# Kernel tuning notes

Measured on AMD Instinct MI355X. Metric: run time of the kernel, lower is better.

## Reference

```python
import jax, jax.numpy as jnp
import numpy as np

# Module hyperparameters (match init_kwargs)
C = 64      # in_channels
O = 256     # out_channels
K = 3       # filter_size
SUB = 2     # subsampling
SIGMA = 1.0
SCALE = 1.0 / SIGMA ** 2
EPS = 1e-8


def setup_inputs() -> dict:
    key = jax.random.key(0)
    k1, k2 = jax.random.split(key)
    x = jax.random.normal(k1, (32, C, 64, 64), dtype=jnp.float32)
    weight = jax.random.normal(k2, (O, C * K * K), dtype=jnp.float32)
    return {"x": x, "weight": weight}


def reference(x, weight):
    # Faithful to CKNLayer.forward, but expressed as a direct convolution
    # instead of materializing the im2col (unfold) tensor:
    #   unfold -> per-patch L2 norm -> (patches/norm) @ w_norm.T
    # == conv(x, w_norm) / patch_norm,   patch_norm = sqrt(conv(x^2, ones))
    B, _, H, W = x.shape
    pad = K // 2

    # F.normalize(weight, p=2, dim=1): clamp norm at 1e-12
    w_norm = weight / jnp.maximum(
        jnp.linalg.norm(weight, axis=1, keepdims=True), 1e-12
    )
    # torch unfold orders patch features as (c, kh, kw) -> reshape matches
    w4 = w_norm.reshape(O, C, K, K)

    dn = jax.lax.conv_dimension_numbers(x.shape, w4.shape, ('NCHW', 'OIHW', 'NCHW'))
    dots = jax.lax.conv_general_dilated(
        x, w4, window_strides=(1, 1), padding=[(pad, pad), (pad, pad)],
        dimension_numbers=dn)  # [B, O, H, W]

    ones_k = jnp.ones((1, C, K, K), x.dtype)
    sq = jax.lax.conv_general_dilated(
        x * x, ones_k, window_strides=(1, 1), padding=[(pad, pad), (pad, pad)],
        dimension_numbers=dn)  # [B, 1, H, W] = sum of squares per patch
    patch_norm = jnp.sqrt(jnp.maximum(sq, 0.0)) + EPS

    # Gaussian RBF on the unit sphere: exp(scale * (cos_sim - 1))
    out = jnp.exp(SCALE * (dots / patch_norm - 1.0))  # [B, O, H, W]

    # avg_pool2d(kernel=SUB, stride=SUB), H, W divisible by SUB
    out = out.reshape(B, O, H // SUB, SUB, W // SUB, SUB).mean(axis=(3, 5))
    return out
```

## Files before the change

### kernel.cpp

```cpp
#include <hip/hip_runtime.h>
#include <hip/hip_bf16.h>

typedef __attribute__((ext_vector_type(8))) short bf16x8;
typedef __attribute__((ext_vector_type(4))) float f32x4;
typedef __attribute__((ext_vector_type(16))) float f32x16;
typedef __attribute__((ext_vector_type(4))) unsigned u32x4;

__device__ __forceinline__ unsigned bfbits(float v) {
  __hip_bfloat16 h = __float2bfloat16(v);
  return (unsigned)*reinterpret_cast<unsigned short*>(&h);
}

__global__ void wnorm_kernel(const float* __restrict__ w,
                             ushort* __restrict__ wt,
                             ushort* __restrict__ wt3) {
  const int o = blockIdx.x;
  const int c = threadIdx.x;
  float v[9];
  float ss = 0.f;
  const float* row = w + o * 576 + c * 9;
#pragma unroll
  for (int j = 0; j < 9; ++j) { v[j] = row[j]; ss += v[j] * v[j]; }
#pragma unroll
  for (int off = 32; off > 0; off >>= 1) ss += __shfl_xor(ss, off);
  const float inv = 1.0f / fmaxf(sqrtf(ss), 1e-12f);
  const int g = o >> 5, n = o & 31;
#pragma unroll
  for (int j = 0; j < 9; ++j) {
    const ushort bv = (ushort)bfbits(v[j] * inv);
    wt[o * 576 + j * 64 + c] = bv;
    const int ks = j * 4 + (c >> 4);
    wt3[((ks * 8 + g) * 32 + n) * 16 + (c & 15)] = bv;
  }
}

__global__ __launch_bounds__(256, 8) void xprep_kernel(
    const float* __restrict__ x, ushort* __restrict__ xt,
    float* __restrict__ css) {
  __shared__ __align__(16) unsigned tile[64 * 33];
  __shared__ __align__(16) float cssp[4 * 64];
  const int t = threadIdx.x;
  const int y = blockIdx.x, b = blockIdx.y;
  const int c = t >> 2, m = t & 3;
  const int lane = t & 63, w = t >> 6;

  const float* src = x + (((size_t)b * 64 + c) * 64 + y) * 64 + m * 4;
  float f[16];
#pragma unroll
  for (int j4 = 0; j4 < 4; ++j4) {
    const f32x4 v = *(const f32x4*)(src + j4 * 16);
#pragma unroll
    for (int k = 0; k < 4; ++k) f[j4 * 4 + k] = v[k];
  }
  float s[16];
#pragma unroll
  for (int j = 0; j < 16; ++j) {
    float v = f[j] * f[j];
    v += __shfl_xor(v, 4);
    v += __shfl_xor(v, 8);
    v += __shfl_xor(v, 16);
    v += __shfl_xor(v, 32);
    s[j] = v;
  }
  if (lane < 4) {
#pragma unroll
    for (int j4 = 0; j4 < 4; ++j4) {
      f32x4 v = {s[j4 * 4], s[j4 * 4 + 1], s[j4 * 4 + 2], s[j4 * 4 + 3]};
      *(f32x4*)(cssp + w * 64 + j4 * 16 + lane * 4) = v;
    }
  }
  const int parity = c & 1;
  const int c2 = c >> 1;
#pragma unroll
  for (int j = 0; j < 16; ++j) {
    const float pf = __shfl_xor(f[j], 4);
    const bool mine = parity ? (j >= 8) : (j < 8);
    if (mine) {
      const unsigned dw = parity ? (bfbits(pf) | (bfbits(f[j]) << 16))
                                 : (bfbits(f[j]) | (bfbits(pf) << 16));
      const int px = (j >> 2) * 16 + m * 4 + (j & 3);
      tile[px * 33 + c2] = dw;
    }
  }
  __syncthreads();
  {
    const int xr = t >> 2, q = t & 3;
    unsigned d[8];
#pragma unroll
    for (int i = 0; i < 8; ++i) d[i] = tile[xr * 33 + q * 8 + i];
    ushort* dst = xt + (((size_t)b * 64 + y) * 64 + xr) * 64 + q * 16;
    u32x4 v0 = {d[0], d[1], d[2], d[3]};
    u32x4 v1 = {d[4], d[5], d[6], d[7]};
    *(u32x4*)dst = v0;
    *(u32x4*)(dst + 8) = v1;
  }
  if (t < 64) {
    const float sum = cssp[t] + cssp[64 + t] + cssp[128 + t] + cssp[192 + t];
    css[((size_t)b * 64 + y) * 64 + t] = sum;
  }
}

__global__ void invp_kernel(const float* __restrict__ css,
                            float* __restrict__ invp) {
  const int xx = threadIdx.x;
  const int y = blockIdx.x, b = blockIdx.y;
  float s = 0.f;
#pragma unroll
  for (int dy = -1; dy <= 1; ++dy) {
    const int yy = y + dy;
    if ((unsigned)yy < 64u) s += css[((size_t)b * 64 + yy) * 64 + xx];
  }
  const float sl = __shfl_up(s, 1);
  const float sr = __shfl_down(s, 1);
  const float tot = s + ((xx > 0) ? sl : 0.f) + ((xx < 63) ? sr : 0.f);
  invp[((size_t)b * 64 + y) * 64 + xx] =
      1.0f / (sqrtf(fmaxf(tot, 0.f)) + 1e-8f);
}

__global__ __launch_bounds__(512, 4) void ckn_main(
    const ushort* __restrict__ xt, const float* __restrict__ invp_g,
    const ushort* __restrict__ wt3, float* __restrict__ out) {
  __shared__ __align__(16) char smem[37376];
  char* const xs = smem;
  float* const pool = (float*)smem;
  float* const invp = (float*)(smem + 36864);

  const int tid = threadIdx.x;
  const int y0 = blockIdx.x;
  const int b = blockIdx.y;

  if (tid < 64) {
    const int r4 = tid >> 4, colsel = (tid >> 3) & 1, cblk = tid & 7;
    *(f32x4*)(xs + r4 * 8448 + colsel * 65 * 128 + cblk * 16) =
        (f32x4){0.f, 0.f, 0.f, 0.f};
  }
  if (tid < 128)
    invp[tid] = invp_g[((size_t)b * 64 + 2 * y0 + (tid >> 6)) * 64 + (tid & 63)];

  {
    const int xx = tid >> 3;
    const int c0 = 8 * ((tid & 7) ^ ((xx + 1) & 7));
    const ushort* srcb = xt + ((size_t)b * 64) * 4096 + (size_t)xx * 64 + c0;
#pragma unroll
    for (int r4 = 0; r4 < 4; ++r4) {
      const int y_img = 2 * y0 - 1 + r4;
      char* dst = xs + r4 * 8448 + 128 + tid * 16;
      if ((unsigned)y_img < 64u) {
        const ushort* src = srcb + (size_t)y_img * 4096;
        __builtin_amdgcn_global_load_lds(
            (const __attribute__((address_space(1))) void*)src,
            (__attribute__((address_space(3))) void*)dst, 16, 0, 0);
      } else {
        *(f32x4*)dst = (f32x4){0.f, 0.f, 0.f, 0.f};
      }
    }
  }

  const int lane = tid & 63;
  const int wid = tid >> 6;
  const int wave_m = wid & 1;
  const int wave_n = wid >> 1;
  const int lane31 = lane & 31;
  const int hi = lane >> 5;

  const ushort* wb3 = wt3 + (size_t)lane31 * 16 + hi * 8;
  const int g0 = wave_n * 2;

  bf16x8 bq[2][2];
#pragma unroll
  for (int nf = 0; nf < 2; ++nf) {
    bq[0][nf] = *(const bf16x8*)(wb3 + (size_t)(0 * 8 + g0 + nf) * 512);
    bq[1][nf] = *(const bf16x8*)(wb3 + (size_t)(1 * 8 + g0 + nf) * 512);
  }

  __syncthreads();

  f32x16 acc[2][2];
#pragma unroll
  for (int i = 0; i < 2; ++i)
#pragma unroll
    for (int j = 0; j < 2; ++j)
#pragma unroll
      for (int e = 0; e < 16; ++e) acc[i][j][e] = 0.f;

#pragma unroll
  for (int ks = 0; ks < 36; ++ks) {
    const int t9 = ks >> 2;
    const int kh = t9 / 3, kw = t9 % 3;
    const int cb = (ks & 3) * 32 + hi * 16;
    const int r4 = wave_m + kh;
    const int cur = ks & 1;
    bf16x8 afrag[2];
#pragma unroll
    for (int mf = 0; mf < 2; ++mf) {
      const int col = mf * 32 + lane31 + kw;
      const int addr = r4 * 8448 + col * 128 + (cb ^ ((col & 7) << 4));
      afrag[mf] = *(const bf16x8*)(xs + addr);
    }
    __builtin_amdgcn_s_setprio(1);
#pragma unroll
    for (int mf = 0; mf < 2; ++mf)
#pragma unroll
      for (int nf = 0; nf < 2; ++nf)
        acc[mf][nf] = __builtin_amdgcn_mfma_f32_32x32x16_bf16(
            afrag[mf], bq[cur][nf], acc[mf][nf], 0, 0, 0);
    __builtin_amdgcn_s_setprio(0);
    if (ks + 2 < 36) {
#pragma unroll
      for (int nf = 0; nf < 2; ++nf)
        bq[cur][nf] =
            *(const bf16x8*)(wb3 + (size_t)((ks + 2) * 8 + g0 + nf) * 512);
    }
  }

  float ep[2][2][4][2];
#pragma unroll
  for (int mf = 0; mf < 2; ++mf) {
#pragma unroll
    for (int q = 0; q < 4; ++q) {
      const f32x4 ip =
          *(const f32x4*)(invp + wave_m * 64 + mf * 32 + 8 * q + 4 * hi);
#pragma unroll
      for (int nf = 0; nf < 2; ++nf) {
        const float e0 = __expf(acc[mf][nf][4 * q + 0] * ip[0] - 1.f);
        const float e1 = __expf(acc[mf][nf][4 * q + 1] * ip[1] - 1.f);
        const float e2 = __expf(acc[mf][nf][4 * q + 2] * ip[2] - 1.f);
        const float e3 = __expf(acc[mf][nf][4 * q + 3] * ip[3] - 1.f);
        ep[mf][nf][q][0] = e0 + e1;
        ep[mf][nf][q][1] = e2 + e3;
      }
    }
  }
  __syncthreads();

  if (wave_m == 1) {
#pragma unroll
    for (int mf = 0; mf < 2; ++mf)
#pragma unroll
      for (int nf = 0; nf < 2; ++nf)
#pragma unroll
        for (int q = 0; q < 4; ++q) {
          const int o = wave_n * 64 + nf * 32 + lane31;
          const int px = mf * 16 + 4 * q + 2 * hi;
          *(float2*)(pool + o * 36 + px) =
              make_float2(ep[mf][nf][q][0], ep[mf][nf][q][1]);
        }
  }
  __syncthreads();
  if (wave_m == 0) {
#pragma unroll
    for (int mf = 0; mf < 2; ++mf)
#pragma unroll
      for (int nf = 0; nf < 2; ++nf)
#pragma unroll
        for (int q = 0; q < 4; ++q) {
          const int o = wave_n * 64 + nf * 32 + lane31;
          const int px = mf * 16 + 4 * q + 2 * hi;
          float2* p = (float2*)(pool + o * 36 + px);
          const float2 othr = *p;
          *p = make_float2(0.25f * (ep[mf][nf][q][0] + othr.x),
                           0.25f * (ep[mf][nf][q][1] + othr.y));
        }
  }
  __syncthreads();

  const size_t obase = (((size_t)b * 256) * 32 + y0) * 32;
#pragma unroll
  for (int j = 0; j < 4; ++j) {
    const int o = j * 64 + (tid >> 3);
    const int ch = (tid & 7) * 4;
    const f32x4 v = *(const f32x4*)(pool + o * 36 + ch);
    *(f32x4*)(out + obase + (size_t)o * 1024 + ch) = v;
  }
}

__global__ __launch_bounds__(512, 4) void ckn_main_v1(
    const float* __restrict__ x, const ushort* __restrict__ wt,
    float* __restrict__ out) {
  __shared__ __align__(16) char smem[43552];
  char* const xs = smem;
  float* const invp = (float*)(smem + 33792);
  float* const cs = (float*)(smem + 34304);
  float* const csp = (float*)(smem + 35360);
  float* const pool = (float*)smem;

  const int tid = threadIdx.x;
  const int y0 = blockIdx.x;
  const int b = blockIdx.y;

  if (tid < 64) {
    const int r4 = tid >> 4, colsel = (tid >> 3) & 1, cblk = tid & 7;
    const int col = colsel * 65;
    *(f32x4*)(xs + r4 * 8448 + col * 128 + cblk * 16) =
        (f32x4){0.f, 0.f, 0.f, 0.f};
  }
  {
    const int xx = tid & 63;
    const int cg = tid >> 6;
    const int col = xx + 1;
    const int sw = (cg * 16) ^ ((col & 7) << 4);
#pragma unroll
    for (int r4 = 0; r4 < 4; ++r4) {
      const int y_img = 2 * y0 - 1 + r4;
      char* dst = xs + r4 * 8448 + col * 128 + sw;
      if ((unsigned)y_img < 64u) {
        const float* src =
            x + (((size_t)b * 64 + cg * 8) * 64 + y_img) * 64 + xx;
        float ss = 0.f;
        union { bf16x8 v; ushort u[8]; } pk;
#pragma unroll
        for (int j = 0; j < 8; ++j) {
          const float f = src[(size_t)j * 4096];
          ss += f * f;
          pk.u[j] = (ushort)bfbits(f);
        }
        *(bf16x8*)dst = pk.v;
        csp[(r4 * 8 + cg) * 64 + xx] = ss;
      } else {
        *(bf16x8*)dst = (bf16x8){0, 0, 0, 0, 0, 0, 0, 0};
        csp[(r4 * 8 + cg) * 64 + xx] = 0.f;
      }
    }
  }
  __syncthreads();
  if (tid < 256) {
    const int r4 = tid >> 6, xc = tid & 63;
    float s = 0.f;
#pragma unroll
    for (int cg = 0; cg < 8; ++cg) s += csp[(r4 * 8 + cg) * 64 + xc];
    cs[r4 * 66 + xc + 1] = s;
  }
  if (tid >= 256 && tid < 264) {
    const int t = tid - 256;
    cs[(t >> 1) * 66 + (t & 1) * 65] = 0.f;
  }
  __syncthreads();
  if (tid < 128) {
    const int ry = tid >> 6, xp = tid & 63;
    float s = 0.f;
#pragma unroll
    for (int dr = 0; dr < 3; ++dr)
#pragma unroll
      for (int dc = 0; dc < 3; ++dc) s += cs[(ry + dr) * 66 + xp + dc];
    invp[tid] = 1.0f / (sqrtf(fmaxf(s, 0.f)) + 1e-8f);
  }
  __syncthreads();

  const int lane = tid & 63;
  const int wid = tid >> 6;
  const int wave_m = wid & 1;
  const int wave_n = wid >> 1;
  const int lane16 = lane & 15;
  const int klane = lane >> 4;
  const int o_base = wave_n * 64;

  f32x4 acc[4][4];
#pragma unroll
  for (int i = 0; i < 4; ++i)
#pragma unroll
    for (int j = 0; j < 4; ++j) acc[i][j] = (f32x4){0.f, 0.f, 0.f, 0.f};
  const ushort* wbase = wt + (o_base + lane16) * 576 + klane * 8;
#pragma unroll
  for (int ks = 0; ks < 18; ++ks) {
    const int t9 = ks >> 1;
    const int kh = t9 / 3, kw = t9 % 3;
    const int cb = (ks & 1) * 64 + klane * 16;
    bf16x8 bfrag[4];
#pragma unroll
    for (int fn = 0; fn < 4; ++fn)
      bfrag[fn] = *(const bf16x8*)(wbase + fn * 16 * 576 + ks * 32);
    const int r4 = wave_m + kh;
#pragma unroll
    for (int fm = 0; fm < 4; ++fm) {
      const int col = fm * 16 + lane16 + kw;
      const int addr = r4 * 8448 + col * 128 + (cb ^ ((col & 7) << 4));
      const bf16x8 afrag = *(const bf16x8*)(xs + addr);
#pragma unroll
      for (int fn = 0; fn < 4; ++fn)
        acc[fm][fn] = __builtin_amdgcn_mfma_f32_16x16x32_bf16(
            afrag, bfrag[fn], acc[fm][fn], 0, 0, 0);
    }
  }
  float ep0[4][4], ep1[4][4];
#pragma unroll
  for (int fm = 0; fm < 4; ++fm) {
    const int m = wave_m * 64 + fm * 16 + klane * 4;
    const f32x4 ip = *(const f32x4*)(invp + m);
#pragma unroll
    for (int fn = 0; fn < 4; ++fn) {
      const f32x4 v = acc[fm][fn];
      const float e0 = __expf(v[0] * ip[0] - 1.f);
      const float e1 = __expf(v[1] * ip[1] - 1.f);
      const float e2 = __expf(v[2] * ip[2] - 1.f);
      const float e3 = __expf(v[3] * ip[3] - 1.f);
      ep0[fm][fn] = e0 + e1;
      ep1[fm][fn] = e2 + e3;
    }
  }
  __syncthreads();
  if (wave_m == 1) {
#pragma unroll
    for (int fm = 0; fm < 4; ++fm) {
      const int ox = fm * 8 + klane * 2;
#pragma unroll
      for (int fn = 0; fn < 4; ++fn) {
        const int o = o_base + fn * 16 + lane16;
        *(float2*)(pool + o * 32 + ox) = make_float2(ep0[fm][fn], ep1[fm][fn]);
      }
    }
  }
  __syncthreads();
  if (wave_m == 0) {
#pragma unroll
    for (int fm = 0; fm < 4; ++fm) {
      const int ox = fm * 8 + klane * 2;
#pragma unroll
      for (int fn = 0; fn < 4; ++fn) {
        const int o = o_base + fn * 16 + lane16;
        const float2 othr = *(const float2*)(pool + o * 32 + ox);
        const float r0 = 0.25f * (ep0[fm][fn] + othr.x);
        const float r1 = 0.25f * (ep1[fm][fn] + othr.y);
        *(float2*)(out + ((((size_t)b * 256 + o) * 32 + y0) * 32 + ox)) =
            make_float2(r0, r1);
      }
    }
  }
}

extern "C" void kernel_launch(void* const* d_in, const int* in_sizes, int n_in,
                              void* d_out, int out_size, void* d_ws,
                              size_t ws_size, hipStream_t stream) {
  const float* x = (const float*)d_in[0];
  const float* w = (const float*)d_in[1];
  float* out = (float*)d_out;

  const size_t XT_BYTES = 32ull * 64 * 64 * 64 * 2;
  const size_t CSS_BYTES = 32ull * 64 * 64 * 4;
  const size_t WT_BYTES = 256ull * 576 * 2;
  const size_t NEED = XT_BYTES + 2 * CSS_BYTES + 2 * WT_BYTES;

  if (ws_size >= NEED) {
    ushort* xt = (ushort*)d_ws;
    float* css = (float*)((char*)d_ws + XT_BYTES);
    float* invp = (float*)((char*)d_ws + XT_BYTES + CSS_BYTES);
    ushort* wt = (ushort*)((char*)d_ws + XT_BYTES + 2 * CSS_BYTES);
    ushort* wt3 = (ushort*)((char*)d_ws + XT_BYTES + 2 * CSS_BYTES + WT_BYTES);

    wnorm_kernel<<<dim3(256), dim3(64), 0, stream>>>(w, wt, wt3);
    xprep_kernel<<<dim3(64, 32), dim3(256), 0, stream>>>(x, xt, css);
    invp_kernel<<<dim3(64, 32), dim3(64), 0, stream>>>(css, invp);
    ckn_main<<<dim3(32, 32), dim3(512), 0, stream>>>(xt, invp, wt3, out);
  } else {
    ushort* wt = (ushort*)d_ws;
    ushort* wt3 = wt + 256 * 576;
    if (ws_size >= 2 * WT_BYTES) {
      wnorm_kernel<<<dim3(256), dim3(64), 0, stream>>>(w, wt, wt3);
      ckn_main_v1<<<dim3(32, 32), dim3(512), 0, stream>>>(x, wt, out);
    }
  }
}
```

Measured before the change: 71.39 us.

## Fuse weight-normalization and patch-norm kernels into neighbours, transpose pool layout

Folds the weight-normalization work into an extra row of xprep blocks and computes the inverse patch norms inside the main kernel from per-pixel channel sums. This cuts the launch count from four to two and drops the invp buffer round trip. The LDS swizzle changes to a two-level XOR, and A-fragment addresses are precomputed per lane so the K loop does less address arithmetic. The pooled tile is stored output-channel-contiguous in a separate LDS region, which raises shared memory to about 66KB and may lower occupancy, and the exp epilogue is merged into the pooling stores.

```diff
diff --git a/kernel.cpp b/kernel.cpp
--- a/kernel.cpp
+++ b/kernel.cpp
@@ -11,11 +11,14 @@
   return (unsigned)*reinterpret_cast<unsigned short*>(&h);
 }
 
-__global__ void wnorm_kernel(const float* __restrict__ w,
-                             ushort* __restrict__ wt,
-                             ushort* __restrict__ wt3) {
-  const int o = blockIdx.x;
-  const int c = threadIdx.x;
+__device__ __forceinline__ int gswz(int col) {
+  return (col & 7) ^ (((col >> 3) & 3) << 1);
+}
+
+__device__ __forceinline__ void wnorm_one(const float* __restrict__ w,
+                                          ushort* __restrict__ wt,
+                                          ushort* __restrict__ wt3,
+                                          int o, int c) {
   float v[9];
   float ss = 0.f;
   const float* row = w + o * 576 + c * 9;
@@ -34,15 +37,26 @@
   }
 }
 
+__global__ void wnorm_kernel(const float* __restrict__ w,
+                             ushort* __restrict__ wt,
+                             ushort* __restrict__ wt3) {
+  wnorm_one(w, wt, wt3, blockIdx.x, threadIdx.x);
+}
+
 __global__ __launch_bounds__(256, 8) void xprep_kernel(
     const float* __restrict__ x, ushort* __restrict__ xt,
-    float* __restrict__ css) {
+    float* __restrict__ css, const float* __restrict__ w,
+    ushort* __restrict__ wt, ushort* __restrict__ wt3) {
   __shared__ __align__(16) unsigned tile[64 * 33];
   __shared__ __align__(16) float cssp[4 * 64];
   const int t = threadIdx.x;
+  if (blockIdx.y == 32) {
+    wnorm_one(w, wt, wt3, blockIdx.x * 4 + (t >> 6), t & 63);
+    return;
+  }
   const int y = blockIdx.x, b = blockIdx.y;
   const int c = t >> 2, m = t & 3;
-  const int lane = t & 63, w = t >> 6;
+  const int lane = t & 63, wv = t >> 6;
 
   const float* src = x + (((size_t)b * 64 + c) * 64 + y) * 64 + m * 4;
   float f[16];
@@ -66,7 +80,7 @@
 #pragma unroll
     for (int j4 = 0; j4 < 4; ++j4) {
       f32x4 v = {s[j4 * 4], s[j4 * 4 + 1], s[j4 * 4 + 2], s[j4 * 4 + 3]};
-      *(f32x4*)(cssp + w * 64 + j4 * 16 + lane * 4) = v;
+      *(f32x4*)(cssp + wv * 64 + j4 * 16 + lane * 4) = v;
     }
   }
   const int parity = c & 1;
@@ -100,46 +114,43 @@
   }
 }
 
-__global__ void invp_kernel(const float* __restrict__ css,
-                            float* __restrict__ invp) {
-  const int xx = threadIdx.x;
-  const int y = blockIdx.x, b = blockIdx.y;
-  float s = 0.f;
-#pragma unroll
-  for (int dy = -1; dy <= 1; ++dy) {
-    const int yy = y + dy;
-    if ((unsigned)yy < 64u) s += css[((size_t)b * 64 + yy) * 64 + xx];
-  }
-  const float sl = __shfl_up(s, 1);
-  const float sr = __shfl_down(s, 1);
-  const float tot = s + ((xx > 0) ? sl : 0.f) + ((xx < 63) ? sr : 0.f);
-  invp[((size_t)b * 64 + y) * 64 + xx] =
-      1.0f / (sqrtf(fmaxf(tot, 0.f)) + 1e-8f);
-}
-
 __global__ __launch_bounds__(512, 4) void ckn_main(
-    const ushort* __restrict__ xt, const float* __restrict__ invp_g,
+    const ushort* __restrict__ xt, const float* __restrict__ css,
     const ushort* __restrict__ wt3, float* __restrict__ out) {
-  __shared__ __align__(16) char smem[37376];
+  __shared__ __align__(16) char smem[67584];
   char* const xs = smem;
-  float* const pool = (float*)smem;
-  float* const invp = (float*)(smem + 36864);
+  float* const pool = (float*)(smem + 33792);
+  float* const invp = (float*)(smem + 67072);
+  const int PS = 260;
 
   const int tid = threadIdx.x;
   const int y0 = blockIdx.x;
   const int b = blockIdx.y;
+
+  if (tid < 128) {
+    const int ry = tid >> 6, xx = tid & 63;
+    const int yc = 2 * y0 + ry;
+    float s = 0.f;
+#pragma unroll
+    for (int dy = -1; dy <= 1; ++dy) {
+      const int yy = yc + dy;
+      if ((unsigned)yy < 64u) s += css[((size_t)b * 64 + yy) * 64 + xx];
+    }
+    const float sl = __shfl_up(s, 1);
+    const float sr = __shfl_down(s, 1);
+    const float tot = s + ((xx > 0) ? sl : 0.f) + ((xx < 63) ? sr : 0.f);
+    invp[tid] = 1.0f / (sqrtf(fmaxf(tot, 0.f)) + 1e-8f);
+  }
 
   if (tid < 64) {
     const int r4 = tid >> 4, colsel = (tid >> 3) & 1, cblk = tid & 7;
     *(f32x4*)(xs + r4 * 8448 + colsel * 65 * 128 + cblk * 16) =
         (f32x4){0.f, 0.f, 0.f, 0.f};
   }
-  if (tid < 128)
-    invp[tid] = invp_g[((size_t)b * 64 + 2 * y0 + (tid >> 6)) * 64 + (tid & 63)];
 
   {
     const int xx = tid >> 3;
-    const int c0 = 8 * ((tid & 7) ^ ((xx + 1) & 7));
+    const int c0 = 8 * ((tid & 7) ^ gswz(xx + 1));
     const ushort* srcb = xt + ((size_t)b * 64) * 4096 + (size_t)xx * 64 + c0;
 #pragma unroll
     for (int r4 = 0; r4 < 4; ++r4) {
@@ -173,6 +184,17 @@
     bq[1][nf] = *(const bf16x8*)(wb3 + (size_t)(1 * 8 + g0 + nf) * 512);
   }
 
+  const int hi16 = hi << 4;
+  int PH[2][3];
+#pragma unroll
+  for (int mf = 0; mf < 2; ++mf)
+#pragma unroll
+    for (int kw = 0; kw < 3; ++kw) {
+      const int col = mf * 32 + lane31 + kw;
+      PH[mf][kw] = (col * 128 + (gswz(col) << 4)) ^ hi16;
+    }
+  const int rb0 = wave_m * 8448;
+
   __syncthreads();
 
   f32x16 acc[2][2];
@@ -187,16 +209,12 @@
   for (int ks = 0; ks < 36; ++ks) {
     const int t9 = ks >> 2;
     const int kh = t9 / 3, kw = t9 % 3;
-    const int cb = (ks & 3) * 32 + hi * 16;
-    const int r4 = wave_m + kh;
+    const int ksc = (ks & 3) << 5;
     const int cur = ks & 1;
     bf16x8 afrag[2];
 #pragma unroll
-    for (int mf = 0; mf < 2; ++mf) {
-      const int col = mf * 32 + lane31 + kw;
-      const int addr = r4 * 8448 + col * 128 + (cb ^ ((col & 7) << 4));
-      afrag[mf] = *(const bf16x8*)(xs + addr);
-    }
+    for (int mf = 0; mf < 2; ++mf)
+      afrag[mf] = *(const bf16x8*)(xs + rb0 + kh * 8448 + (PH[mf][kw] ^ ksc));
     __builtin_amdgcn_s_setprio(1);
 #pragma unroll
     for (int mf = 0; mf < 2; ++mf)
@@ -213,54 +231,44 @@
     }
   }
 
-  float ep[2][2][4][2];
-#pragma unroll
-  for (int mf = 0; mf < 2; ++mf) {
-#pragma unroll
-    for (int q = 0; q < 4; ++q) {
-      const f32x4 ip =
-          *(const f32x4*)(invp + wave_m * 64 + mf * 32 + 8 * q + 4 * hi);
-#pragma unroll
-      for (int nf = 0; nf < 2; ++nf) {
-        const float e0 = __expf(acc[mf][nf][4 * q + 0] * ip[0] - 1.f);
-        const float e1 = __expf(acc[mf][nf][4 * q + 1] * ip[1] - 1.f);
-        const float e2 = __expf(acc[mf][nf][4 * q + 2] * ip[2] - 1.f);
-        const float e3 = __expf(acc[mf][nf][4 * q + 3] * ip[3] - 1.f);
-        ep[mf][nf][q][0] = e0 + e1;
-        ep[mf][nf][q][1] = e2 + e3;
-      }
-    }
-  }
-  __syncthreads();
-
   if (wave_m == 1) {
 #pragma unroll
     for (int mf = 0; mf < 2; ++mf)
 #pragma unroll
-      for (int nf = 0; nf < 2; ++nf)
-#pragma unroll
-        for (int q = 0; q < 4; ++q) {
+      for (int q = 0; q < 4; ++q) {
+        const f32x4 ip = *(const f32x4*)(invp + 64 + mf * 32 + 8 * q + 4 * hi);
+        const int px = mf * 16 + 4 * q + 2 * hi;
+#pragma unroll
+        for (int nf = 0; nf < 2; ++nf) {
           const int o = wave_n * 64 + nf * 32 + lane31;
-          const int px = mf * 16 + 4 * q + 2 * hi;
-          *(float2*)(pool + o * 36 + px) =
-              make_float2(ep[mf][nf][q][0], ep[mf][nf][q][1]);
+          const float e0 = __expf(acc[mf][nf][4 * q + 0] * ip[0] - 1.f);
+          const float e1 = __expf(acc[mf][nf][4 * q + 1] * ip[1] - 1.f);
+          const float e2 = __expf(acc[mf][nf][4 * q + 2] * ip[2] - 1.f);
+          const float e3 = __expf(acc[mf][nf][4 * q + 3] * ip[3] - 1.f);
+          pool[px * PS + o] = e0 + e1;
+          pool[(px + 1) * PS + o] = e2 + e3;
         }
+      }
   }
   __syncthreads();
   if (wave_m == 0) {
 #pragma unroll
     for (int mf = 0; mf < 2; ++mf)
 #pragma unroll
-      for (int nf = 0; nf < 2; ++nf)
-#pragma unroll
-        for (int q = 0; q < 4; ++q) {
+      for (int q = 0; q < 4; ++q) {
+        const f32x4 ip = *(const f32x4*)(invp + mf * 32 + 8 * q + 4 * hi);
+        const int px = mf * 16 + 4 * q + 2 * hi;
+#pragma unroll
+        for (int nf = 0; nf < 2; ++nf) {
           const int o = wave_n * 64 + nf * 32 + lane31;
-          const int px = mf * 16 + 4 * q + 2 * hi;
-          float2* p = (float2*)(pool + o * 36 + px);
-          const float2 othr = *p;
-          *p = make_float2(0.25f * (ep[mf][nf][q][0] + othr.x),
-                           0.25f * (ep[mf][nf][q][1] + othr.y));
+          const float e0 = __expf(acc[mf][nf][4 * q + 0] * ip[0] - 1.f);
+          const float e1 = __expf(acc[mf][nf][4 * q + 1] * ip[1] - 1.f);
+          const float e2 = __expf(acc[mf][nf][4 * q + 2] * ip[2] - 1.f);
+          const float e3 = __expf(acc[mf][nf][4 * q + 3] * ip[3] - 1.f);
+          pool[px * PS + o] = 0.25f * (pool[px * PS + o] + e0 + e1);
+          pool[(px + 1) * PS + o] = 0.25f * (pool[(px + 1) * PS + o] + e2 + e3);
         }
+      }
   }
   __syncthreads();
 
@@ -269,7 +277,8 @@
   for (int j = 0; j < 4; ++j) {
     const int o = j * 64 + (tid >> 3);
     const int ch = (tid & 7) * 4;
-    const f32x4 v = *(const f32x4*)(pool + o * 36 + ch);
+    const f32x4 v = {pool[(ch + 0) * PS + o], pool[(ch + 1) * PS + o],
+                     pool[(ch + 2) * PS + o], pool[(ch + 3) * PS + o]};
     *(f32x4*)(out + obase + (size_t)o * 1024 + ch) = v;
   }
 }
@@ -437,19 +446,17 @@
   const size_t XT_BYTES = 32ull * 64 * 64 * 64 * 2;
   const size_t CSS_BYTES = 32ull * 64 * 64 * 4;
   const size_t WT_BYTES = 256ull * 576 * 2;
-  const size_t NEED = XT_BYTES + 2 * CSS_BYTES + 2 * WT_BYTES;
+  const size_t NEED = XT_BYTES + CSS_BYTES + 2 * WT_BYTES;
 
   if (ws_size >= NEED) {
     ushort* xt = (ushort*)d_ws;
     float* css = (float*)((char*)d_ws + XT_BYTES);
-    float* invp = (float*)((char*)d_ws + XT_BYTES + CSS_BYTES);
-    ushort* wt = (ushort*)((char*)d_ws + XT_BYTES + 2 * CSS_BYTES);
-    ushort* wt3 = (ushort*)((char*)d_ws + XT_BYTES + 2 * CSS_BYTES + WT_BYTES);
-
-    wnorm_kernel<<<dim3(256), dim3(64), 0, stream>>>(w, wt, wt3);
-    xprep_kernel<<<dim3(64, 32), dim3(256), 0, stream>>>(x, xt, css);
-    invp_kernel<<<dim3(64, 32), dim3(64), 0, stream>>>(css, invp);
-    ckn_main<<<dim3(32, 32), dim3(512), 0, stream>>>(xt, invp, wt3, out);
+    ushort* wt = (ushort*)((char*)d_ws + XT_BYTES + CSS_BYTES);
+    ushort* wt3 = (ushort*)((char*)d_ws + XT_BYTES + CSS_BYTES + WT_BYTES);
+
+    xprep_kernel<<<dim3(64, 33), dim3(256), 0, stream>>>(x, xt, css, w, wt,
+                                                         wt3);
+    ckn_main<<<dim3(32, 32), dim3(512), 0, stream>>>(xt, css, wt3, out);
   } else {
     ushort* wt = (ushort*)d_ws;
     ushort* wt3 = wt + 256 * 576;
```

Result: faster. 65.81 us (-7.8%).
